# Kernel optimization log

Measured on AMD Instinct MI355X. Metric: run time of the kernel, lower is better.

## Reference

```python
import jax, jax.numpy as jnp
import numpy as np

N = 50000   # num_nodes
E = 800000  # edges for relation 0
DIN = 512
DOUT = 128


def setup_inputs() -> dict:
    key = jax.random.key(0)
    k1, k2, k3 = jax.random.split(key, 3)
    x = jax.random.normal(k1, (N, DIN), dtype=jnp.float32)
    edge_index = jax.random.randint(k2, (2, E), 0, N, dtype=jnp.int64)
    # GCNConv weight (glorot-ish) and zero bias, as after reset_parameters()
    W = jax.random.normal(k3, (DIN, DOUT), dtype=jnp.float32) * (1.0 / np.sqrt(DIN))
    b = jnp.zeros((DOUT,), dtype=jnp.float32)
    return {"x": x, "edge_index": edge_index, "W": W, "b": b,
            "dropout_probability": 0.5}


def _dropout(h, key, p):
    keep = jax.random.bernoulli(key, 1.0 - p, h.shape)
    return jnp.where(keep, h / (1.0 - p), jnp.zeros((), h.dtype))


def _gcn_conv(h, edge_index, W, b):
    # PyG GCNConv: add self-loops, symmetric normalization, XW then scatter-add.
    src, dst = edge_index[0], edge_index[1]
    loops = jnp.arange(N, dtype=src.dtype)
    col = jnp.concatenate([src, loops])  # gather side (source)
    row = jnp.concatenate([dst, loops])  # scatter side (target)
    ones = jnp.ones(row.shape[0], dtype=h.dtype)
    deg = jax.ops.segment_sum(ones, row, num_segments=N)        # in-degree + 1
    dinv = jnp.where(deg > 0, jax.lax.rsqrt(deg), jnp.zeros((), h.dtype))
    norm = dinv[row] * dinv[col]                                # [E+N]
    hw = h @ W                                                  # [N, DOUT] dense GEMM
    msg = hw[col] * norm[:, None]                               # gather + scale
    out = jax.ops.segment_sum(msg, row, num_segments=N)         # scatter-add
    return out + b


def reference(x, edge_index, W, b, dropout_probability):
    # Forward loop in the source breaks after the first relation, so exactly one
    # conv is applied. training=True dropout with fixed keys for determinism.
    p = dropout_probability
    k1, k2, k3 = jax.random.split(jax.random.key(1), 3)

    pos_seq = _dropout(x, k1, p)
    pos_h = jax.nn.relu(_gcn_conv(pos_seq, edge_index, W, b))
    summary = jax.nn.sigmoid(jnp.mean(pos_h, axis=0, keepdims=True))

    neg_seq = _dropout(x, k2, p)
    perm = jax.random.permutation(k3, N)   # torch.randperm corruption
    neg_h = jax.nn.relu(_gcn_conv(neg_seq[perm], edge_index, W, b))

    return (pos_h, neg_h, summary, pos_seq, neg_seq)
```

## Files before the change

kernel.cpp:

```cpp
#include <hip/hip_runtime.h>
#include <stdint.h>

static constexpr int    N_NODES = 50000;
static constexpr int    N_EDGES = 800000;
static constexpr int    DIN     = 512;
static constexpr int    DOUT    = 128;
static constexpr size_t SEQ_ELEMS = (size_t)N_NODES * DIN;
static constexpr size_t H_ELEMS   = (size_t)N_NODES * DOUT;

static constexpr int RS_NB = 49;
static constexpr int EDGE_BLOCKS = 782;
static_assert(N_NODES % 8 == 0, "gather grid assumes 8 nodes/block exactly");

typedef __attribute__((ext_vector_type(8))) short bf16x8;
typedef __attribute__((ext_vector_type(4))) float f32x4;
typedef __attribute__((ext_vector_type(4))) unsigned short u16x4;
typedef __attribute__((ext_vector_type(8))) unsigned short u16x8;

static constexpr size_t W_HDR    = 0;
static constexpr size_t W_DEGCNT = 16;
static constexpr size_t W_CURSOR = 50016;
static constexpr size_t W_SUMBUF = 100016;
static constexpr size_t W_CNT    = 100144;
static constexpr size_t W_ZEND   = 100152;
static constexpr size_t W_HIST   = 100152;
static constexpr size_t W_OFFS   = 150328;
static constexpr size_t W_ROWPTR = 175416;
static constexpr size_t W_COLSRC = 225420;
static constexpr size_t W_DINV   = 1025420;
static constexpr size_t W_KEYS   = 1075420;
static constexpr size_t W_VALS   = 1275420;
static constexpr size_t W_RANK   = 1475420;
static constexpr size_t W_BT     = 1625420;
static constexpr size_t W_HWI    = 1658188;

__device__ __forceinline__ uint16_t f2bf(float f) {
  uint32_t u = __float_as_uint(f);
  return (uint16_t)((u + 0x7FFFu + ((u >> 16) & 1u)) >> 16);
}
__device__ __forceinline__ float b2f(uint16_t h) {
  return __uint_as_float(((uint32_t)h) << 16);
}
__device__ __forceinline__ uint32_t rotl32(uint32_t x, int r) {
  return (x << r) | (x >> (32 - r));
}

__device__ __forceinline__ void threefry2x32(uint32_t k0, uint32_t k1,
                                             uint32_t x0, uint32_t x1,
                                             uint32_t& o0, uint32_t& o1) {
  uint32_t ks0 = k0, ks1 = k1, ks2 = k0 ^ k1 ^ 0x1BD11BDAu;
  x0 += ks0; x1 += ks1;
#define TF_ROUND(r) { x0 += x1; x1 = rotl32(x1, (r)); x1 ^= x0; }
  TF_ROUND(13) TF_ROUND(15) TF_ROUND(26) TF_ROUND(6)
  x0 += ks1; x1 += ks2 + 1u;
  TF_ROUND(17) TF_ROUND(29) TF_ROUND(16) TF_ROUND(24)
  x0 += ks2; x1 += ks0 + 2u;
  TF_ROUND(13) TF_ROUND(15) TF_ROUND(26) TF_ROUND(6)
  x0 += ks0; x1 += ks1 + 3u;
  TF_ROUND(17) TF_ROUND(29) TF_ROUND(16) TF_ROUND(24)
  x0 += ks1; x1 += ks2 + 4u;
  TF_ROUND(13) TF_ROUND(15) TF_ROUND(26) TF_ROUND(6)
  x0 += ks2; x1 += ks0 + 5u;
#undef TF_ROUND
  o0 = x0; o1 = x1;
}

__device__ __forceinline__ uint32_t randbits32(uint32_t k0, uint32_t k1, uint32_t ctr) {
  uint32_t a, b;
  threefry2x32(k0, k1, 0u, ctr, a, b);
  return a ^ b;
}

__global__ void __launch_bounds__(256) wt_init_kernel(const float* __restrict__ W,
                                                      uint32_t* __restrict__ wsu) {
  {
    int gid = blockIdx.x * 256 + threadIdx.x;
    for (size_t i = W_DEGCNT + gid; i < W_ZEND; i += 4096) wsu[i] = 0u;
  }
  if (blockIdx.x == 0 && threadIdx.x == 0) {
    uint32_t k3a, k3b, ra, rb, s1a, s1b, s2a, s2b;
    threefry2x32(0u, 1u, 0u, 2u, k3a, k3b);
    threefry2x32(k3a, k3b, 0u, 0u, ra, rb);
    threefry2x32(k3a, k3b, 0u, 1u, s1a, s1b);
    threefry2x32(ra, rb, 0u, 1u, s2a, s2b);
    wsu[4] = s1a; wsu[5] = s1b; wsu[6] = s2a; wsu[7] = s2b;
  }
  uint16_t* BT = (uint16_t*)(wsu + W_BT);
  __shared__ float tile[32][129];
  int k0 = blockIdx.x * 32;
  int t = threadIdx.x;
  for (int i = t; i < 32 * 128; i += 256) {
    int k = i >> 7, n = i & 127;
    tile[k][n] = W[(size_t)(k0 + k) * DOUT + n];
  }
  __syncthreads();
  for (int i = t; i < 32 * 128; i += 256) {
    int n = i >> 5, k = i & 31;
    BT[(size_t)n * DIN + k0 + k] = f2bf(tile[k][n]);
  }
}

__global__ void __launch_bounds__(1024) fusedA_kernel(const int* __restrict__ ei,
                                                      uint32_t* __restrict__ wsu) {
  int b = blockIdx.x;
  if (b < EDGE_BLOCKS) {
    int e = b * 1024 + threadIdx.x;
    if (e < N_EDGES) atomicAdd(&wsu[W_DEGCNT + ei[N_EDGES + e]], 1u);
  } else {
    __shared__ uint32_t h[256];
    int sb = b - EDGE_BLOCKS, s = sb / RS_NB, bb = sb % RS_NB;
    int t = threadIdx.x;
    if (t < 256) h[t] = 0u;
    __syncthreads();
    uint32_t k0 = wsu[4 + 2 * s], k1 = wsu[5 + 2 * s];
    int p = bb * 1024 + t;
    if (p < N_NODES) {
      uint32_t kv = randbits32(k0, k1, (uint32_t)p);
      wsu[W_KEYS + (size_t)s * 100000 + p] = kv;
      wsu[W_VALS + (size_t)s * 100000 + p] = (uint32_t)p;
      atomicAdd(&h[kv & 255u], 1u);
    }
    __syncthreads();
    if (t < 256) wsu[W_HIST + (size_t)s * 25088 + t * RS_NB + bb] = h[t];
  }
}

__device__ __forceinline__ void scan12544(const uint32_t* __restrict__ hist,
                                          uint32_t* __restrict__ offs,
                                          uint32_t* __restrict__ zeroT,
                                          uint32_t* __restrict__ sc) {
  const int t = threadIdx.x;
  int c0 = t * 13, c1 = c0 + 13;
  if (c0 > 12544) c0 = 12544;
  if (c1 > 12544) c1 = 12544;
  uint32_t loc[13];
  uint32_t sum = 0;
  for (int c = c0; c < c1; ++c) {
    uint32_t v = hist[c];
    loc[c - c0] = v;
    sum += v;
  }
  sc[t] = sum;
  __syncthreads();
  for (int off = 1; off < 1024; off <<= 1) {
    uint32_t xx = (t >= off) ? sc[t - off] : 0u;
    __syncthreads();
    sc[t] += xx;
    __syncthreads();
  }
  uint32_t run = sc[t] - sum;
  for (int c = c0; c < c1; ++c) {
    offs[c] = run;
    run += loc[c - c0];
  }
  if (zeroT != nullptr)
    for (int i = t; i < 12544; i += 1024) zeroT[i] = 0u;
}

__global__ void __launch_bounds__(1024) fusedB_kernel(uint32_t* __restrict__ wsu) {
  __shared__ uint32_t sc[1024];
  int b = blockIdx.x, t = threadIdx.x;
  if (b == 0) {
    int c0 = t * 49, c1 = c0 + 49;
    if (c0 > N_NODES) c0 = N_NODES;
    if (c1 > N_NODES) c1 = N_NODES;
    float* dinv = (float*)(wsu + W_DINV);
    uint32_t sum = 0;
    for (int c = c0; c < c1; ++c) {
      uint32_t v = wsu[W_DEGCNT + c];
      dinv[c] = __frsqrt_rn((float)(v + 1u));
      sum += v;
    }
    sc[t] = sum;
    __syncthreads();
    for (int off = 1; off < 1024; off <<= 1) {
      uint32_t xx = (t >= off) ? sc[t - off] : 0u;
      __syncthreads();
      sc[t] += xx;
      __syncthreads();
    }
    uint32_t run = sc[t] - sum;
    for (int c = c0; c < c1; ++c) {
      uint32_t h = wsu[W_DEGCNT + c];
      wsu[W_ROWPTR + c] = run;
      run += h;
    }
    if (t == 0) wsu[W_ROWPTR + N_NODES] = (uint32_t)N_EDGES;
  } else {
    int s = b - 1;
    scan12544(wsu + W_HIST + (size_t)s * 25088, wsu + W_OFFS + (size_t)s * 12544,
              wsu + W_HIST + (size_t)s * 25088 + 12544, sc);
  }
}

template <int PASS>
__device__ __forceinline__ void scatter_body(int s, int bb, uint32_t* __restrict__ wsu,
                                             uint32_t* __restrict__ gh) {
  const int t = threadIdx.x;
  constexpr int shift = PASS * 8;
  const uint32_t* ki = wsu + W_KEYS + (size_t)s * 100000 + (PASS & 1) * 50000;
  const uint32_t* vi = wsu + W_VALS + (size_t)s * 100000 + (PASS & 1) * 50000;
  uint32_t* ko = wsu + W_KEYS + (size_t)s * 100000 + ((PASS + 1) & 1) * 50000;
  uint32_t* vo = wsu + W_VALS + (size_t)s * 100000 + ((PASS + 1) & 1) * 50000;
  const uint32_t* offs = wsu + W_OFFS + (size_t)s * 12544;
  uint32_t* histN = wsu + W_HIST + (size_t)s * 25088 + ((PASS + 1) & 1) * 12544;
  uint32_t* rank = wsu + W_RANK + (size_t)s * 50000;

  for (int i = t; i < 4096; i += 1024) gh[i] = 0u;
  __syncthreads();
  const int w = t >> 6, l = t & 63;
  const uint64_t pre = (1ull << l) - 1ull;
  int p = bb * 1024 + t;
  bool valid = p < N_NODES;
  uint32_t kv = valid ? ki[p] : 0u;
  uint32_t d = (kv >> shift) & 255u;
  uint64_t m = __ballot(valid);
#pragma unroll
  for (int bit = 0; bit < 8; ++bit) {
    uint64_t bbm = __ballot((d >> bit) & 1u);
    m &= ((d >> bit) & 1u) ? bbm : ~bbm;
  }
  int peer = __popcll(m & pre);
  if (valid && peer == 0) gh[w * 256 + d] = (uint32_t)__popcll(m);
  __syncthreads();
  if (t < 256) {
    uint32_t run = 0;
#pragma unroll
    for (int g = 0; g < 16; ++g) {
      uint32_t tmp = gh[g * 256 + t];
      gh[g * 256 + t] = run;
      run += tmp;
    }
  }
  __syncthreads();
  if (valid) {
    uint32_t pos = offs[d * RS_NB + bb] + gh[w * 256 + d] + (uint32_t)peer;
    uint32_t pv = vi[p];
    if constexpr (PASS == 3) {
      if (pv < (uint32_t)N_NODES && pos < (uint32_t)N_NODES)
        rank[pv] = pos;
    } else {
      if (pos < (uint32_t)N_NODES) {
        ko[pos] = kv;
        vo[pos] = pv;
        atomicAdd(&histN[((kv >> (shift + 8)) & 255u) * RS_NB + (pos >> 10)], 1u);
      }
    }
  }
}

__global__ void __launch_bounds__(1024) fusedC_kernel(const int* __restrict__ ei,
                                                      uint32_t* __restrict__ wsu) {
  __shared__ uint32_t gh[4096];
  int b = blockIdx.x;
  if (b < EDGE_BLOCKS) {
    int e = b * 1024 + threadIdx.x;
    if (e < N_EDGES) {
      int src = ei[e], dst = ei[N_EDGES + e];
      uint32_t pos = wsu[W_ROWPTR + dst] + atomicAdd(&wsu[W_CURSOR + dst], 1u);
      wsu[W_COLSRC + pos] = (uint32_t)src;
    }
  } else {
    int sb = b - EDGE_BLOCKS;
    scatter_body<0>(sb / RS_NB, sb % RS_NB, wsu, gh);
  }
}

template <int PASS>
__global__ void __launch_bounds__(1024) scat_kernel(uint32_t* __restrict__ wsu) {
  __shared__ uint32_t gh[4096];
  int b = blockIdx.x;
  scatter_body<PASS>(b / RS_NB, b % RS_NB, wsu, gh);
}

template <int PASS>
__global__ void __launch_bounds__(1024) scan_kernel(uint32_t* __restrict__ wsu) {
  __shared__ uint32_t sc[1024];
  int s = blockIdx.x;
  const uint32_t* h = wsu + W_HIST + (size_t)s * 25088 + (PASS & 1) * 12544;
  uint32_t* of = wsu + W_OFFS + (size_t)s * 12544;
  uint32_t* z = (PASS < 3) ? (wsu + W_HIST + (size_t)s * 25088 + ((PASS + 1) & 1) * 12544)
                           : nullptr;
  scan12544(h, of, z, sc);
}

__global__ void __launch_bounds__(256) dg_kernel(const float* __restrict__ x,
                                                 const uint16_t* __restrict__ BT,
                                                 const float* __restrict__ pprob,
                                                 const float* __restrict__ dinv,
                                                 const uint32_t* __restrict__ rankA,
                                                 const uint32_t* __restrict__ rankB,
                                                 float* __restrict__ seq_pos,
                                                 float* __restrict__ seq_neg,
                                                 uint16_t* __restrict__ hwI, int M) {
  __shared__ __align__(16) uint16_t ldsA[64 * 64];
  __shared__ __align__(16) uint16_t ldsB[128 * 64];
  const int which = blockIdx.y;
  float* seq = which ? seq_neg : seq_pos;

  uint32_t kk0, kk1;
  threefry2x32(0u, 1u, 0u, (uint32_t)which, kk0, kk1);
  const float p = pprob[0];
  const float keep_p = 1.0f - p;
  const float scale  = 1.0f / keep_p;
  uint32_t Tint = (uint32_t)ceilf(keep_p * 8388608.0f);
  uint32_t Tu = (Tint >= (1u << 23)) ? 0xFFFFFFFFu : (Tint << 9);

  const int tid  = threadIdx.x;
  const int lane = tid & 63;
  const int w    = tid >> 6;
  const int wr   = w >> 1, wc = w & 1;
  const int m0   = blockIdx.x * 64;
  const int l15  = lane & 15, l4 = lane >> 4;
  const int lr   = lane >> 3, lk = (lane & 7) * 8;

  f32x4 acc[2][4] = {};

  for (int k0 = 0; k0 < DIN; k0 += 64) {
#pragma unroll
    for (int s = 0; s < 4; ++s) {
      int nbase = w * 32 + s * 8;
      const uint16_t* gp = BT + (size_t)(nbase + lr) * DIN + k0 + lk;
      __builtin_amdgcn_global_load_lds(
          (const __attribute__((address_space(1))) void*)gp,
          (__attribute__((address_space(3))) void*)(ldsB + nbase * 64), 16, 0, 0);
    }
    __builtin_amdgcn_sched_barrier(0);
#pragma unroll
    for (int i = 0; i < 4; ++i) {
      int idx = tid + i * 256;
      int row = idx >> 4, q = idx & 15;
      int grow = m0 + row;
      int crow = (grow < M) ? grow : (M - 1);
      float4 v = *reinterpret_cast<const float4*>(x + (size_t)crow * DIN + k0 + q * 4);
      float r[4] = {v.x, v.y, v.z, v.w};
      uint32_t cbase = (uint32_t)crow * DIN + k0 + q * 4;
#pragma unroll
      for (int j = 0; j < 4; ++j) {
        uint32_t bits = randbits32(kk0, kk1, cbase + j);
        r[j] = (bits < Tu) ? r[j] * scale : 0.0f;
      }
      *reinterpret_cast<float4*>(seq + (size_t)crow * DIN + k0 + q * 4) =
          make_float4(r[0], r[1], r[2], r[3]);
      uint32_t u0 = __float_as_uint(r[0]), u1 = __float_as_uint(r[1]);
      uint32_t lo = (u0 >> 16) | (u1 & 0xFFFF0000u);
      u0 = __float_as_uint(r[2]); u1 = __float_as_uint(r[3]);
      uint32_t hi = (u0 >> 16) | (u1 & 0xFFFF0000u);
      *reinterpret_cast<uint2*>(&ldsA[row * 64 + q * 4]) = make_uint2(lo, hi);
    }
    asm volatile("s_waitcnt vmcnt(4) lgkmcnt(0)" ::: "memory");
    __builtin_amdgcn_s_barrier();
    __builtin_amdgcn_sched_barrier(0);
#pragma unroll
    for (int kk = 0; kk < 2; ++kk) {
      bf16x8 afr[2], bfr[4];
#pragma unroll
      for (int f = 0; f < 2; ++f)
        afr[f] = *reinterpret_cast<const bf16x8*>(ldsA + (wr * 32 + f * 16 + l15) * 64 + kk * 32 + l4 * 8);
#pragma unroll
      for (int f = 0; f < 4; ++f)
        bfr[f] = *reinterpret_cast<const bf16x8*>(ldsB + (wc * 64 + f * 16 + l15) * 64 + kk * 32 + l4 * 8);
#pragma unroll
      for (int fm = 0; fm < 2; ++fm)
#pragma unroll
        for (int fn = 0; fn < 4; ++fn)
          acc[fm][fn] = __builtin_amdgcn_mfma_f32_16x16x32_bf16(afr[fm], bfr[fn], acc[fm][fn], 0, 0, 0);
    }
    __builtin_amdgcn_s_barrier();
  }
#pragma unroll
  for (int fm = 0; fm < 2; ++fm) {
#pragma unroll
    for (int r = 0; r < 4; ++r) {
      int row = m0 + wr * 32 + fm * 16 + l4 * 4 + r;
      if (row < M) {
        uint32_t slot = (uint32_t)row;
        if (which) {
          uint32_t r1 = rankA[row];
          slot = (r1 < (uint32_t)N_NODES) ? rankB[r1] : 0u;
          if (slot >= (uint32_t)N_NODES) slot = 0u;
        }
        float sc = dinv[slot];
        uint16_t* cp = hwI + (size_t)slot * 256 + which * 128 + wc * 64 + l15;
#pragma unroll
        for (int fn = 0; fn < 4; ++fn)
          cp[fn * 16] = f2bf(acc[fm][fn][r] * sc);
      }
    }
  }
}

__global__ void __launch_bounds__(256) gcn_gather_kernel(const uint16_t* __restrict__ hwI,
                                                         const float* __restrict__ dinv,
                                                         const uint32_t* __restrict__ rowptr,
                                                         const uint32_t* __restrict__ colsrc,
                                                         const float* __restrict__ bias,
                                                         float* __restrict__ out_pos,
                                                         float* __restrict__ out_neg) {
  const int t = threadIdx.x;
  int node = blockIdx.x * 8 + (t >> 5);
  int lane32 = t & 31;
  int c8 = (lane32 & 15) * 8;
  int half = lane32 >> 4;
  uint32_t e0 = rowptr[node], e1 = rowptr[node + 1];
  float a0 = 0.f, a1 = 0.f, a2 = 0.f, a3 = 0.f, a4 = 0.f, a5 = 0.f, a6 = 0.f, a7 = 0.f;
  uint32_t e = e0;
  for (; e + 8 <= e1; e += 8) {
    uint32_t ss[8];
#pragma unroll
    for (int j = 0; j < 8; ++j) ss[j] = colsrc[e + j];
    u16x8 vv[8];
#pragma unroll
    for (int j = 0; j < 8; ++j)
      vv[j] = *reinterpret_cast<const u16x8*>(hwI + (size_t)ss[j] * 256 + lane32 * 8);
#pragma unroll
    for (int j = 0; j < 8; ++j) {
      a0 += b2f(vv[j][0]); a1 += b2f(vv[j][1]); a2 += b2f(vv[j][2]); a3 += b2f(vv[j][3]);
      a4 += b2f(vv[j][4]); a5 += b2f(vv[j][5]); a6 += b2f(vv[j][6]); a7 += b2f(vv[j][7]);
    }
  }
  for (; e < e1; ++e) {
    uint32_t s = colsrc[e];
    u16x8 v = *reinterpret_cast<const u16x8*>(hwI + (size_t)s * 256 + lane32 * 8);
    a0 += b2f(v[0]); a1 += b2f(v[1]); a2 += b2f(v[2]); a3 += b2f(v[3]);
    a4 += b2f(v[4]); a5 += b2f(v[5]); a6 += b2f(v[6]); a7 += b2f(v[7]);
  }
  u16x8 sv = *reinterpret_cast<const u16x8*>(hwI + (size_t)node * 256 + lane32 * 8);
  float dn = dinv[node];
  float4 b0 = *reinterpret_cast<const float4*>(bias + c8);
  float4 b1 = *reinterpret_cast<const float4*>(bias + c8 + 4);
  float4 o0, o1;
  o0.x = fmaxf(dn * (a0 + b2f(sv[0])) + b0.x, 0.0f);
  o0.y = fmaxf(dn * (a1 + b2f(sv[1])) + b0.y, 0.0f);
  o0.z = fmaxf(dn * (a2 + b2f(sv[2])) + b0.z, 0.0f);
  o0.w = fmaxf(dn * (a3 + b2f(sv[3])) + b0.w, 0.0f);
  o1.x = fmaxf(dn * (a4 + b2f(sv[4])) + b1.x, 0.0f);
  o1.y = fmaxf(dn * (a5 + b2f(sv[5])) + b1.y, 0.0f);
  o1.z = fmaxf(dn * (a6 + b2f(sv[6])) + b1.z, 0.0f);
  o1.w = fmaxf(dn * (a7 + b2f(sv[7])) + b1.w, 0.0f);
  float* dst = (half ? out_neg : out_pos) + (size_t)node * DOUT + c8;
  *reinterpret_cast<float4*>(dst)     = o0;
  *reinterpret_cast<float4*>(dst + 4) = o1;
}

__global__ void __launch_bounds__(128) colsum_sig_kernel(const float* __restrict__ ph,
                                                         float* __restrict__ sumbuf,
                                                         uint32_t* __restrict__ counter,
                                                         float* __restrict__ outs) {
  int c = threadIdx.x;
  int r0 = blockIdx.x * 256;
  int r1 = r0 + 256; if (r1 > N_NODES) r1 = N_NODES;
  float s = 0.0f;
  for (int r = r0; r < r1; ++r) s += ph[(size_t)r * DOUT + c];
  atomicAdd(&sumbuf[c], s);
  __threadfence();
  __syncthreads();
  __shared__ uint32_t lastflag;
  if (c == 0) lastflag = atomicAdd(counter, 1u);
  __syncthreads();
  if (lastflag == gridDim.x - 1) {
    __threadfence();
    float m = atomicAdd(&sumbuf[c], 0.0f) * (1.0f / (float)N_NODES);
    outs[c] = 1.0f / (1.0f + expf(-m));
  }
}

extern "C" void kernel_launch(void* const* d_in, const int* in_sizes, int n_in,
                              void* d_out, int out_size, void* d_ws, size_t ws_size,
                              hipStream_t stream) {
  const float* x     = (const float*)d_in[0];
  const int*   ei    = (const int*)d_in[1];
  const float* W     = (const float*)d_in[2];
  const float* bias  = (const float*)d_in[3];
  const float* pprob = (const float*)d_in[4];

  float* out = (float*)d_out;
  float* out_pos_h   = out;
  float* out_neg_h   = out + H_ELEMS;
  float* out_summary = out + 2 * H_ELEMS;
  float* out_pos_seq = out + 2 * H_ELEMS + DOUT;
  float* out_neg_seq = out_pos_seq + SEQ_ELEMS;

  uint32_t* wsu    = (uint32_t*)d_ws;
  float*    sumbuf = (float*)(wsu + W_SUMBUF);
  uint32_t* rowptr = wsu + W_ROWPTR;
  uint32_t* colsrc = wsu + W_COLSRC;
  float*    dinv   = (float*)(wsu + W_DINV);
  uint32_t* rankA  = wsu + W_RANK;
  uint32_t* rankB  = wsu + W_RANK + 50000;
  uint16_t* BT     = (uint16_t*)(wsu + W_BT);
  uint16_t* hwI    = (uint16_t*)(wsu + W_HWI);

  wt_init_kernel<<<DIN / 32, 256, 0, stream>>>(W, wsu);

  fusedA_kernel<<<EDGE_BLOCKS + 2 * RS_NB, 1024, 0, stream>>>(ei, wsu);

  fusedB_kernel<<<3, 1024, 0, stream>>>(wsu);

  fusedC_kernel<<<EDGE_BLOCKS + 2 * RS_NB, 1024, 0, stream>>>(ei, wsu);

  scan_kernel<1><<<2, 1024, 0, stream>>>(wsu);
  scat_kernel<1><<<2 * RS_NB, 1024, 0, stream>>>(wsu);
  scan_kernel<2><<<2, 1024, 0, stream>>>(wsu);
  scat_kernel<2><<<2 * RS_NB, 1024, 0, stream>>>(wsu);
  scan_kernel<3><<<2, 1024, 0, stream>>>(wsu);
  scat_kernel<3><<<2 * RS_NB, 1024, 0, stream>>>(wsu);

  dim3 dgrid((N_NODES + 63) / 64, 2);
  dg_kernel<<<dgrid, 256, 0, stream>>>(x, BT, pprob, dinv, rankA, rankB,
                                       out_pos_seq, out_neg_seq, hwI, N_NODES);

  gcn_gather_kernel<<<N_NODES / 8, 256, 0, stream>>>(hwI, dinv, rowptr, colsrc,
                                                     bias, out_pos_h, out_neg_h);

  colsum_sig_kernel<<<(N_NODES + 255) / 256, 128, 0, stream>>>(out_pos_h, sumbuf,
                                                               wsu + W_CNT + 3, out_summary);

  (void)in_sizes; (void)n_in; (void)out_size; (void)ws_size;
}
```

Baseline: 554.9 us.

## Load W fragments directly from global and double-buffer A tile to drop barrier

The B (weight) operand fragments are now read straight from global memory into registers instead of being staged through LDS with global_load_lds. The A tile is double-buffered in LDS, which removes the trailing barrier in each k-iteration. This cuts LDS traffic and sync points in the fused dropout+GEMM kernel, at the cost of more global loads of W (mostly L2-resident) and higher register pressure.

```diff
diff --git a/kernel.cpp b/kernel.cpp
--- a/kernel.cpp
+++ b/kernel.cpp
@@ -293,8 +293,7 @@
                                                  float* __restrict__ seq_pos,
                                                  float* __restrict__ seq_neg,
                                                  uint16_t* __restrict__ hwI, int M) {
-  __shared__ __align__(16) uint16_t ldsA[64 * 64];
-  __shared__ __align__(16) uint16_t ldsB[128 * 64];
+  __shared__ __align__(16) uint16_t ldsA[2][64 * 64];
   const int which = blockIdx.y;
   float* seq = which ? seq_neg : seq_pos;
 
@@ -312,20 +311,19 @@
   const int wr   = w >> 1, wc = w & 1;
   const int m0   = blockIdx.x * 64;
   const int l15  = lane & 15, l4 = lane >> 4;
-  const int lr   = lane >> 3, lk = (lane & 7) * 8;
 
   f32x4 acc[2][4] = {};
 
-  for (int k0 = 0; k0 < DIN; k0 += 64) {
-#pragma unroll
-    for (int s = 0; s < 4; ++s) {
-      int nbase = w * 32 + s * 8;
-      const uint16_t* gp = BT + (size_t)(nbase + lr) * DIN + k0 + lk;
-      __builtin_amdgcn_global_load_lds(
-          (const __attribute__((address_space(1))) void*)gp,
-          (__attribute__((address_space(3))) void*)(ldsB + nbase * 64), 16, 0, 0);
-    }
-    __builtin_amdgcn_sched_barrier(0);
+  int kb = 0;
+  for (int k0 = 0; k0 < DIN; k0 += 64, kb ^= 1) {
+    bf16x8 bfr[2][4];
+#pragma unroll
+    for (int kk = 0; kk < 2; ++kk)
+#pragma unroll
+      for (int f = 0; f < 4; ++f)
+        bfr[kk][f] = *reinterpret_cast<const bf16x8*>(
+            BT + (size_t)(wc * 64 + f * 16 + l15) * DIN + k0 + kk * 32 + l4 * 8);
+
 #pragma unroll
     for (int i = 0; i < 4; ++i) {
       int idx = tid + i * 256;
@@ -346,27 +344,24 @@
       uint32_t lo = (u0 >> 16) | (u1 & 0xFFFF0000u);
       u0 = __float_as_uint(r[2]); u1 = __float_as_uint(r[3]);
       uint32_t hi = (u0 >> 16) | (u1 & 0xFFFF0000u);
-      *reinterpret_cast<uint2*>(&ldsA[row * 64 + q * 4]) = make_uint2(lo, hi);
-    }
-    asm volatile("s_waitcnt vmcnt(4) lgkmcnt(0)" ::: "memory");
+      *reinterpret_cast<uint2*>(&ldsA[kb][row * 64 + q * 4]) = make_uint2(lo, hi);
+    }
+    asm volatile("s_waitcnt lgkmcnt(0)" ::: "memory");
     __builtin_amdgcn_s_barrier();
     __builtin_amdgcn_sched_barrier(0);
 #pragma unroll
     for (int kk = 0; kk < 2; ++kk) {
-      bf16x8 afr[2], bfr[4];
+      bf16x8 afr[2];
 #pragma unroll
       for (int f = 0; f < 2; ++f)
-        afr[f] = *reinterpret_cast<const bf16x8*>(ldsA + (wr * 32 + f * 16 + l15) * 64 + kk * 32 + l4 * 8);
-#pragma unroll
-      for (int f = 0; f < 4; ++f)
-        bfr[f] = *reinterpret_cast<const bf16x8*>(ldsB + (wc * 64 + f * 16 + l15) * 64 + kk * 32 + l4 * 8);
+        afr[f] = *reinterpret_cast<const bf16x8*>(
+            &ldsA[kb][(wr * 32 + f * 16 + l15) * 64 + kk * 32 + l4 * 8]);
 #pragma unroll
       for (int fm = 0; fm < 2; ++fm)
 #pragma unroll
         for (int fn = 0; fn < 4; ++fn)
-          acc[fm][fn] = __builtin_amdgcn_mfma_f32_16x16x32_bf16(afr[fm], bfr[fn], acc[fm][fn], 0, 0, 0);
-    }
-    __builtin_amdgcn_s_barrier();
+          acc[fm][fn] = __builtin_amdgcn_mfma_f32_16x16x32_bf16(afr[fm], bfr[kk][fn], acc[fm][fn], 0, 0, 0);
+    }
   }
 #pragma unroll
   for (int fm = 0; fm < 2; ++fm) {
```

Result: no change. 563.2 us (+1.5%).

## Replace four-pass LSD radix sort for permutation with bucket sort plus in-bucket ranking

Applied to the files above, without the earlier changes.

The four-pass 8-bit LSD radix sort that computes the random permutation ranks is replaced by one 16-bit bucket histogram with global atomics, a scan, an atomic bucket scatter, and a per-bucket O(c^2) rank kernel. This removes six small serialized kernel launches (three scan/scatter pairs) and their syncs. In exchange it relies on buckets staying small; the count is capped at 64 per bucket, and the atomic scatter order is non-deterministic, though the rank uses key and index comparisons and stays exact.

```diff
diff --git a/kernel.cpp b/kernel.cpp
--- a/kernel.cpp
+++ b/kernel.cpp
@@ -23,8 +23,6 @@
 static constexpr size_t W_SUMBUF = 100016;
 static constexpr size_t W_CNT    = 100144;
 static constexpr size_t W_ZEND   = 100152;
-static constexpr size_t W_HIST   = 100152;
-static constexpr size_t W_OFFS   = 150328;
 static constexpr size_t W_ROWPTR = 175416;
 static constexpr size_t W_COLSRC = 225420;
 static constexpr size_t W_DINV   = 1025420;
@@ -33,6 +31,9 @@
 static constexpr size_t W_RANK   = 1475420;
 static constexpr size_t W_BT     = 1625420;
 static constexpr size_t W_HWI    = 1658188;
+static constexpr size_t W_BHIST  = 8058188;
+static constexpr size_t W_BOFF   = 8189260;
+static constexpr size_t W_BCUR   = 8320332;
 
 __device__ __forceinline__ uint16_t f2bf(float f) {
   uint32_t u = __float_as_uint(f);
@@ -76,6 +77,7 @@
   {
     int gid = blockIdx.x * 256 + threadIdx.x;
     for (size_t i = W_DEGCNT + gid; i < W_ZEND; i += 4096) wsu[i] = 0u;
+    for (size_t i = W_BHIST + gid; i < W_BHIST + 131072; i += 4096) wsu[i] = 0u;
   }
   if (blockIdx.x == 0 && threadIdx.x == 0) {
     uint32_t k3a, k3b, ra, rb, s1a, s1b, s2a, s2b;
@@ -107,54 +109,14 @@
     int e = b * 1024 + threadIdx.x;
     if (e < N_EDGES) atomicAdd(&wsu[W_DEGCNT + ei[N_EDGES + e]], 1u);
   } else {
-    __shared__ uint32_t h[256];
     int sb = b - EDGE_BLOCKS, s = sb / RS_NB, bb = sb % RS_NB;
-    int t = threadIdx.x;
-    if (t < 256) h[t] = 0u;
-    __syncthreads();
-    uint32_t k0 = wsu[4 + 2 * s], k1 = wsu[5 + 2 * s];
-    int p = bb * 1024 + t;
+    int p = bb * 1024 + threadIdx.x;
     if (p < N_NODES) {
-      uint32_t kv = randbits32(k0, k1, (uint32_t)p);
+      uint32_t kv = randbits32(wsu[4 + 2 * s], wsu[5 + 2 * s], (uint32_t)p);
       wsu[W_KEYS + (size_t)s * 100000 + p] = kv;
-      wsu[W_VALS + (size_t)s * 100000 + p] = (uint32_t)p;
-      atomicAdd(&h[kv & 255u], 1u);
-    }
-    __syncthreads();
-    if (t < 256) wsu[W_HIST + (size_t)s * 25088 + t * RS_NB + bb] = h[t];
-  }
-}
-
-__device__ __forceinline__ void scan12544(const uint32_t* __restrict__ hist,
-                                          uint32_t* __restrict__ offs,
-                                          uint32_t* __restrict__ zeroT,
-                                          uint32_t* __restrict__ sc) {
-  const int t = threadIdx.x;
-  int c0 = t * 13, c1 = c0 + 13;
-  if (c0 > 12544) c0 = 12544;
-  if (c1 > 12544) c1 = 12544;
-  uint32_t loc[13];
-  uint32_t sum = 0;
-  for (int c = c0; c < c1; ++c) {
-    uint32_t v = hist[c];
-    loc[c - c0] = v;
-    sum += v;
-  }
-  sc[t] = sum;
-  __syncthreads();
-  for (int off = 1; off < 1024; off <<= 1) {
-    uint32_t xx = (t >= off) ? sc[t - off] : 0u;
-    __syncthreads();
-    sc[t] += xx;
-    __syncthreads();
-  }
-  uint32_t run = sc[t] - sum;
-  for (int c = c0; c < c1; ++c) {
-    offs[c] = run;
-    run += loc[c - c0];
-  }
-  if (zeroT != nullptr)
-    for (int i = t; i < 12544; i += 1024) zeroT[i] = 0u;
+      atomicAdd(&wsu[W_BHIST + (size_t)s * 65536 + (kv >> 16)], 1u);
+    }
+  }
 }
 
 __global__ void __launch_bounds__(1024) fusedB_kernel(uint32_t* __restrict__ wsu) {
@@ -188,70 +150,32 @@
     if (t == 0) wsu[W_ROWPTR + N_NODES] = (uint32_t)N_EDGES;
   } else {
     int s = b - 1;
-    scan12544(wsu + W_HIST + (size_t)s * 25088, wsu + W_OFFS + (size_t)s * 12544,
-              wsu + W_HIST + (size_t)s * 25088 + 12544, sc);
-  }
-}
-
-template <int PASS>
-__device__ __forceinline__ void scatter_body(int s, int bb, uint32_t* __restrict__ wsu,
-                                             uint32_t* __restrict__ gh) {
-  const int t = threadIdx.x;
-  constexpr int shift = PASS * 8;
-  const uint32_t* ki = wsu + W_KEYS + (size_t)s * 100000 + (PASS & 1) * 50000;
-  const uint32_t* vi = wsu + W_VALS + (size_t)s * 100000 + (PASS & 1) * 50000;
-  uint32_t* ko = wsu + W_KEYS + (size_t)s * 100000 + ((PASS + 1) & 1) * 50000;
-  uint32_t* vo = wsu + W_VALS + (size_t)s * 100000 + ((PASS + 1) & 1) * 50000;
-  const uint32_t* offs = wsu + W_OFFS + (size_t)s * 12544;
-  uint32_t* histN = wsu + W_HIST + (size_t)s * 25088 + ((PASS + 1) & 1) * 12544;
-  uint32_t* rank = wsu + W_RANK + (size_t)s * 50000;
-
-  for (int i = t; i < 4096; i += 1024) gh[i] = 0u;
-  __syncthreads();
-  const int w = t >> 6, l = t & 63;
-  const uint64_t pre = (1ull << l) - 1ull;
-  int p = bb * 1024 + t;
-  bool valid = p < N_NODES;
-  uint32_t kv = valid ? ki[p] : 0u;
-  uint32_t d = (kv >> shift) & 255u;
-  uint64_t m = __ballot(valid);
-#pragma unroll
-  for (int bit = 0; bit < 8; ++bit) {
-    uint64_t bbm = __ballot((d >> bit) & 1u);
-    m &= ((d >> bit) & 1u) ? bbm : ~bbm;
-  }
-  int peer = __popcll(m & pre);
-  if (valid && peer == 0) gh[w * 256 + d] = (uint32_t)__popcll(m);
-  __syncthreads();
-  if (t < 256) {
-    uint32_t run = 0;
-#pragma unroll
-    for (int g = 0; g < 16; ++g) {
-      uint32_t tmp = gh[g * 256 + t];
-      gh[g * 256 + t] = run;
-      run += tmp;
-    }
-  }
-  __syncthreads();
-  if (valid) {
-    uint32_t pos = offs[d * RS_NB + bb] + gh[w * 256 + d] + (uint32_t)peer;
-    uint32_t pv = vi[p];
-    if constexpr (PASS == 3) {
-      if (pv < (uint32_t)N_NODES && pos < (uint32_t)N_NODES)
-        rank[pv] = pos;
-    } else {
-      if (pos < (uint32_t)N_NODES) {
-        ko[pos] = kv;
-        vo[pos] = pv;
-        atomicAdd(&histN[((kv >> (shift + 8)) & 255u) * RS_NB + (pos >> 10)], 1u);
-      }
+    const uint32_t* bh = wsu + W_BHIST + (size_t)s * 65536;
+    uint32_t* boff = wsu + W_BOFF + (size_t)s * 65536;
+    uint32_t* bcur = wsu + W_BCUR + (size_t)s * 65536;
+    int c0 = t * 64;
+    uint32_t sum = 0;
+    for (int j = 0; j < 64; ++j) sum += bh[c0 + j];
+    sc[t] = sum;
+    __syncthreads();
+    for (int off = 1; off < 1024; off <<= 1) {
+      uint32_t xx = (t >= off) ? sc[t - off] : 0u;
+      __syncthreads();
+      sc[t] += xx;
+      __syncthreads();
+    }
+    uint32_t run = sc[t] - sum;
+    for (int j = 0; j < 64; ++j) {
+      uint32_t h = bh[c0 + j];
+      boff[c0 + j] = run;
+      bcur[c0 + j] = run;
+      run += h;
     }
   }
 }
 
 __global__ void __launch_bounds__(1024) fusedC_kernel(const int* __restrict__ ei,
                                                       uint32_t* __restrict__ wsu) {
-  __shared__ uint32_t gh[4096];
   int b = blockIdx.x;
   if (b < EDGE_BLOCKS) {
     int e = b * 1024 + threadIdx.x;
@@ -261,27 +185,42 @@
       wsu[W_COLSRC + pos] = (uint32_t)src;
     }
   } else {
-    int sb = b - EDGE_BLOCKS;
-    scatter_body<0>(sb / RS_NB, sb % RS_NB, wsu, gh);
-  }
-}
-
-template <int PASS>
-__global__ void __launch_bounds__(1024) scat_kernel(uint32_t* __restrict__ wsu) {
-  __shared__ uint32_t gh[4096];
-  int b = blockIdx.x;
-  scatter_body<PASS>(b / RS_NB, b % RS_NB, wsu, gh);
-}
-
-template <int PASS>
-__global__ void __launch_bounds__(1024) scan_kernel(uint32_t* __restrict__ wsu) {
-  __shared__ uint32_t sc[1024];
-  int s = blockIdx.x;
-  const uint32_t* h = wsu + W_HIST + (size_t)s * 25088 + (PASS & 1) * 12544;
-  uint32_t* of = wsu + W_OFFS + (size_t)s * 12544;
-  uint32_t* z = (PASS < 3) ? (wsu + W_HIST + (size_t)s * 25088 + ((PASS + 1) & 1) * 12544)
-                           : nullptr;
-  scan12544(h, of, z, sc);
+    int sb = b - EDGE_BLOCKS, s = sb / RS_NB, bb = sb % RS_NB;
+    int p = bb * 1024 + threadIdx.x;
+    if (p < N_NODES) {
+      uint32_t kv = wsu[W_KEYS + (size_t)s * 100000 + p];
+      uint32_t pos = atomicAdd(&wsu[W_BCUR + (size_t)s * 65536 + (kv >> 16)], 1u);
+      if (pos < (uint32_t)N_NODES) {
+        wsu[W_KEYS + (size_t)s * 100000 + 50000 + pos] = kv;
+        wsu[W_VALS + (size_t)s * 50000 + pos] = (uint32_t)p;
+      }
+    }
+  }
+}
+
+__global__ void __launch_bounds__(1024) rank_kernel(uint32_t* __restrict__ wsu) {
+  int gid = blockIdx.x * 1024 + threadIdx.x;
+  int s = gid >> 16;
+  int bkt = gid & 65535;
+  uint32_t start = wsu[W_BOFF + (size_t)s * 65536 + bkt];
+  uint32_t end   = wsu[W_BCUR + (size_t)s * 65536 + bkt];
+  if (end > (uint32_t)N_NODES) end = (uint32_t)N_NODES;
+  if (end <= start) return;
+  uint32_t c = end - start;
+  if (c > 64u) c = 64u;
+  const uint32_t* bk = wsu + W_KEYS + (size_t)s * 100000 + 50000;
+  const uint32_t* bv = wsu + W_VALS + (size_t)s * 50000;
+  uint32_t* rank = wsu + W_RANK + (size_t)s * 50000;
+  for (uint32_t i = 0; i < c; ++i) {
+    uint32_t ki = bk[start + i], vi = bv[start + i];
+    uint32_t rib = 0;
+    for (uint32_t j = 0; j < c; ++j) {
+      uint32_t kj = bk[start + j], vj = bv[start + j];
+      rib += (kj < ki) || (kj == ki && vj < vi);
+    }
+    if (vi < (uint32_t)N_NODES && start + rib < (uint32_t)N_NODES)
+      rank[vi] = start + rib;
+  }
 }
 
 __global__ void __launch_bounds__(256) dg_kernel(const float* __restrict__ x,
@@ -499,12 +438,7 @@
 
   fusedC_kernel<<<EDGE_BLOCKS + 2 * RS_NB, 1024, 0, stream>>>(ei, wsu);
 
-  scan_kernel<1><<<2, 1024, 0, stream>>>(wsu);
-  scat_kernel<1><<<2 * RS_NB, 1024, 0, stream>>>(wsu);
-  scan_kernel<2><<<2, 1024, 0, stream>>>(wsu);
-  scat_kernel<2><<<2 * RS_NB, 1024, 0, stream>>>(wsu);
-  scan_kernel<3><<<2, 1024, 0, stream>>>(wsu);
-  scat_kernel<3><<<2 * RS_NB, 1024, 0, stream>>>(wsu);
+  rank_kernel<<<128, 1024, 0, stream>>>(wsu);
 
   dim3 dgrid((N_NODES + 63) / 64, 2);
   dg_kernel<<<dgrid, 256, 0, stream>>>(x, BT, pprob, dinv, rankA, rankB,
```

After: 515.6 us. 7.1% less time.
